# Optimization experiments

Measured on AMD Instinct MI355X. Metric: run time of the kernel, lower is better.

The kernel has to match this reference:

```python
import jax, jax.numpy as jnp
import numpy as np

HIGHWAY_BIAS = 0.0
# SRU rescale=True scales the highway residual to preserve variance:
# scale_x = sqrt(1 + exp(2*highway_bias)) = sqrt(2) for highway_bias=0
SCALE_X = float(np.sqrt(1.0 + np.exp(2.0 * HIGHWAY_BIAS)))
D = 128  # SRU hidden size


def sru_layer(x, W, v, b):
    """One SRU layer. x: (T,B,din); W: (din,k*D) with k=4 if din!=D else 3;
    v: (2,D) recurrent gate weights; b: (2,D) gate biases."""
    T, B, din = x.shape
    k = W.shape[1] // D
    U = jnp.einsum('tbi,ij->tbj', x, W).reshape(T, B, k, D)
    u0, u1, u2 = U[:, :, 0], U[:, :, 1], U[:, :, 2]
    res = U[:, :, 3] if k == 4 else x  # highway residual (projected if dims differ)
    vf, vr = v[0], v[1]
    bf, br = b[0], b[1]

    def step(c, inp):
        u0t, u1t, u2t, rt = inp
        f = jax.nn.sigmoid(u1t + vf * c + bf)          # forget gate (peeks at c_{t-1})
        c_new = f * c + (1.0 - f) * u0t                # cell update
        r = jax.nn.sigmoid(u2t + vr * c_new + br)      # reset/highway gate
        h = r * c_new + (1.0 - r) * rt * SCALE_X       # highway output
        return c_new, h

    c0 = jnp.zeros((B, D), x.dtype)
    _, h = jax.lax.scan(step, c0, (u0, u1, u2, res))
    return h  # (T,B,D)


def sru_stack(x, W0, v0, b0, W1, v1, b1):
    return sru_layer(sru_layer(x, W0, v0, b0), W1, v1, b1)


def setup_inputs() -> dict:
    key = jax.random.key(0)
    ks = jax.random.split(key, 20)
    B, T = 8, 32000
    s_in = 1.0 / np.sqrt(64.0)
    s_hid = 1.0 / np.sqrt(128.0)
    inp = {
        'tensor': jax.random.normal(ks[0], (B, 9, T), jnp.float32),
        'W_first': jax.random.normal(ks[1], (128, 9), jnp.float32) / 3.0,
        'b_first': jnp.zeros((128,), jnp.float32),
        'W_last': jax.random.normal(ks[2], (1, 128), jnp.float32) * s_hid,
        'b_last': jnp.zeros((1,), jnp.float32),
        # stack a = self.lstm2 (processes channels [:64])
        'a_W0': jax.random.normal(ks[3], (64, 4 * D), jnp.float32) * s_in,
        'a_v0': jax.random.normal(ks[4], (2, D), jnp.float32) * 0.1,
        'a_b0': jnp.zeros((2, D), jnp.float32),
        'a_W1': jax.random.normal(ks[5], (D, 3 * D), jnp.float32) * s_hid,
        'a_v1': jax.random.normal(ks[6], (2, D), jnp.float32) * 0.1,
        'a_b1': jnp.zeros((2, D), jnp.float32),
        # stack b = self.lstm (processes channels [64:])
        'b_W0': jax.random.normal(ks[7], (64, 4 * D), jnp.float32) * s_in,
        'b_v0': jax.random.normal(ks[8], (2, D), jnp.float32) * 0.1,
        'b_b0': jnp.zeros((2, D), jnp.float32),
        'b_W1': jax.random.normal(ks[9], (D, 3 * D), jnp.float32) * s_hid,
        'b_v1': jax.random.normal(ks[10], (2, D), jnp.float32) * 0.1,
        'b_b1': jnp.zeros((2, D), jnp.float32),
    }
    return inp


def reference(tensor, W_first, b_first, W_last, b_last,
              a_W0, a_v0, a_b0, a_W1, a_v1, a_b1,
              b_W0, b_v0, b_b0, b_W1, b_v1, b_b1):
    # first: Conv1d(9,128,1)
    h = jnp.einsum('oc,bct->bot', W_first, tensor) + b_first[None, :, None]  # (B,128,T)
    xa = jnp.transpose(h[:, :64], (2, 0, 1))   # (T,B,64) -> lstm2
    xb = jnp.transpose(h[:, 64:], (2, 0, 1))   # (T,B,64) -> lstm
    ya = sru_stack(xa, a_W0, a_v0, a_b0, a_W1, a_v1, a_b1)  # (T,B,128)
    yb = sru_stack(xb, b_W0, b_v0, b_b0, b_W1, b_v1, b_b1)
    s = jnp.transpose(ya + yb, (1, 2, 0))      # (B,128,T)
    # last: Conv1d(128,1,1)
    return jnp.einsum('oc,bct->bot', W_last, s) + b_last[None, :, None]  # (B,1,T)
```

## Files before the change

### kernel.cpp

```cpp
#include <hip/hip_runtime.h>
#include <hip/hip_bf16.h>

#define L2E   1.44269504088896340736f
#define SQRT2 1.41421356237309504880f

#define T_LEN 32000
#define BATCH 8
#define NCH   9

#define KCH0  125
#define CL0   256
#define WU    128
#define KCH1  32
#define CL1   1000
#define WUF   136
#define NTIL  71

#define MROWS (T_LEN*BATCH)

typedef __bf16 bf16x8 __attribute__((ext_vector_type(8)));
typedef float  f32x4  __attribute__((ext_vector_type(4)));
typedef float  f32x2  __attribute__((ext_vector_type(2)));

__global__ void prep_misc(const float* __restrict__ Wf, const float* __restrict__ bfirst,
                          const float* __restrict__ aW0, const float* __restrict__ bW0,
                          const float* __restrict__ ab0, const float* __restrict__ bb0,
                          const float* __restrict__ ab1, const float* __restrict__ bb1,
                          float* __restrict__ Mn, float* __restrict__ biasn,
                          float* __restrict__ bias1n) {
    int s = blockIdx.x, g = blockIdx.y;
    int d = threadIdx.x;
    const float* W0s = s ? bW0 : aW0;
    const float* b0s = s ? bb0 : ab0;
    const float* b1s = s ? bb1 : ab1;

    float scale = (g == 1 || g == 2) ? -L2E : (g == 3 ? SQRT2 : 1.0f);
    float bias = 0.f;
    for (int i = 0; i < 64; ++i) bias += bfirst[s*64 + i] * W0s[i*512 + g*128 + d];
    for (int c = 0; c < NCH; ++c) {
        float acc = 0.f;
        for (int i = 0; i < 64; ++i)
            acc += Wf[(s*64 + i)*NCH + c] * W0s[i*512 + g*128 + d];
        Mn[((s*NCH + c)*4 + g)*128 + d] = scale * acc;
    }
    float bb = bias;
    if (g == 1) bb = bias + b0s[d];
    if (g == 2) bb = bias + b0s[128 + d];
    biasn[(s*4 + g)*128 + d] = scale * bb;

    if (g == 0) {
        bias1n[s*384 + d      ] = 0.0f;
        bias1n[s*384 + 128 + d] = -L2E * b1s[d];
        bias1n[s*384 + 256 + d] = -L2E * b1s[128 + d];
    }
}

__global__ void prep_bpack(const float* __restrict__ aW1, const float* __restrict__ bW1,
                           __hip_bfloat16* __restrict__ Bpack) {
    int nt = blockIdx.x, s = blockIdx.y;
    int kt = threadIdx.x >> 6, lane = threadIdx.x & 63;
    const float* W1s = s ? bW1 : aW1;
    int n = nt*16 + (lane & 15);
    float csc = (n < 128) ? 1.0f : -L2E;
    for (int jj = 0; jj < 8; ++jj) {
        int k = kt*32 + (lane >> 4)*8 + jj;
        Bpack[((size_t)((s*24 + nt)*4 + kt)*64 + lane)*8 + jj] =
            __float2bfloat16(csc * W1s[k*384 + n]);
    }
}

__global__ __launch_bounds__(256, 4) void scan0(const float* __restrict__ tensor,
        const float* __restrict__ av0, const float* __restrict__ bv0,
        const float* __restrict__ Mn, const float* __restrict__ biasn,
        __hip_bfloat16* __restrict__ h0) {
    __shared__ __align__(16) float ldsx[(CL0 + WU) * 12];
    int chunk = blockIdx.x, b = blockIdx.y;
    int tid = threadIdx.x, wid = tid >> 6, lane = tid & 63;
    int s = wid >> 1, half = wid & 1, d = half*64 + lane;

    int t0 = chunk*CL0 - WU; if (t0 < 0) t0 = 0;
    int tend = (chunk + 1)*CL0;
    int nsteps = tend - t0;

    for (int c = 0; c < NCH; ++c) {
        const float* src = tensor + ((size_t)b*NCH + c)*T_LEN + t0;
        for (int j = tid; j < nsteps; j += 256) ldsx[j*12 + c] = src[j];
    }
    __syncthreads();

    f32x2 M01[NCH], M23[NCH], b01, b23;
    {
        float M[4][NCH], bi[4];
#pragma unroll
        for (int g = 0; g < 4; ++g) {
            bi[g] = biasn[(s*4 + g)*128 + d];
#pragma unroll
            for (int c = 0; c < NCH; ++c) M[g][c] = Mn[((s*NCH + c)*4 + g)*128 + d];
        }
#pragma unroll
        for (int c = 0; c < NCH; ++c) {
            M01[c] = (f32x2){M[0][c], M[1][c]};
            M23[c] = (f32x2){M[2][c], M[3][c]};
        }
        b01 = (f32x2){bi[0], bi[1]};
        b23 = (f32x2){bi[2], bi[3]};
    }
    const float* v0s = s ? bv0 : av0;
    float vf2 = -L2E * v0s[d];
    float vr2 = -L2E * v0s[128 + d];

    float cst = 0.f;
    int hw_off = chunk*CL0 - t0;
    __hip_bfloat16* hbase = h0 + ((size_t)s*MROWS + b)*128 + d;

    auto compU = [&](int grp, f32x2* u01v, f32x2* u23v) {
#pragma unroll
        for (int k = 0; k < 4; ++k) {
            const float* xr = ldsx + (grp*4 + k)*12;
            float4 xlo = *(const float4*)xr;
            float4 xhi = *(const float4*)(xr + 4);
            float x8 = xr[8];
            f32x2 a = b01, c2 = b23;
            a += M01[0]*xlo.x; c2 += M23[0]*xlo.x;
            a += M01[1]*xlo.y; c2 += M23[1]*xlo.y;
            a += M01[2]*xlo.z; c2 += M23[2]*xlo.z;
            a += M01[3]*xlo.w; c2 += M23[3]*xlo.w;
            a += M01[4]*xhi.x; c2 += M23[4]*xhi.x;
            a += M01[5]*xhi.y; c2 += M23[5]*xhi.y;
            a += M01[6]*xhi.z; c2 += M23[6]*xhi.z;
            a += M01[7]*xhi.w; c2 += M23[7]*xhi.w;
            a += M01[8]*x8;    c2 += M23[8]*x8;
            u01v[k] = a; u23v[k] = c2;
        }
    };
    auto chain = [&](f32x2* u01v, f32x2* u23v, int grp) {
#pragma unroll
        for (int k = 0; k < 4; ++k) {
            float e  = __builtin_amdgcn_exp2f(fmaf(vf2, cst, u01v[k].y));
            float g  = __builtin_amdgcn_rcpf(e + 1.0f);
            float cn = fmaf(g, cst - u01v[k].x, u01v[k].x);
            float er = __builtin_amdgcn_exp2f(fmaf(vr2, cn, u23v[k].x));
            float rr = __builtin_amdgcn_rcpf(er + 1.0f);
            float h  = fmaf(rr, cn - u23v[k].y, u23v[k].y);
            cst = cn;
            int j = grp*4 + k;
            if (j >= hw_off) hbase[(size_t)(t0 + j)*(BATCH*128)] = __float2bfloat16(h);
        }
    };

    f32x2 uA01[4], uA23[4], uB01[4], uB23[4];
    int ngrp = nsteps >> 2;
    compU(0, uA01, uA23);
    int g = 0;
    while (g + 2 <= ngrp) {
        compU(g + 1, uB01, uB23);
        chain(uA01, uA23, g);
        if (g + 2 < ngrp) compU(g + 2, uA01, uA23);
        chain(uB01, uB23, g + 1);
        g += 2;
    }
}

__global__ __launch_bounds__(768, 3) void scan1f(const __hip_bfloat16* __restrict__ h0,
        const __hip_bfloat16* __restrict__ Bpack, const float* __restrict__ bias1n,
        const float* __restrict__ av1, const float* __restrict__ bv1,
        const float* __restrict__ Wlast, float* __restrict__ pbuf) {
    __shared__ __align__(16) float ush[2][2][16][388];
    __shared__ unsigned int hstg[2][2][16][64];
    int chunk = blockIdx.x, b = blockIdx.y;
    int tid = threadIdx.x, wid = tid >> 6, lane = tid & 63;
    int cl = lane & 15, rsel = lane >> 4;
    int tw = chunk*CL1, t0 = tw - WUF;
    int pp = 0;

    if (wid >= 4) {
        int gw = wid - 4;
        int s_g = gw >> 2;
        int ntb = (gw & 3) * 6;
        bool hwr = ((gw & 3) == 0);
        bf16x8 Bfr[6][4];
        const bf16x8* bsrc = (const bf16x8*)Bpack;
#pragma unroll
        for (int i = 0; i < 6; ++i)
#pragma unroll
            for (int kt = 0; kt < 4; ++kt)
                Bfr[i][kt] = bsrc[((s_g*24 + ntb + i)*4 + kt)*64 + lane];
        float bias[6];
#pragma unroll
        for (int i = 0; i < 6; ++i) bias[i] = bias1n[s_g*384 + (ntb + i)*16 + cl];

        const __hip_bfloat16* habase = h0 + ((size_t)s_g*MROWS + b)*128 + rsel*8;
        bf16x8 A[4];
        auto loadA = [&](int tile) {
            int trow = t0 + tile*16 + cl; if (trow < 0) trow = 0;
            const __hip_bfloat16* ap = habase + (size_t)trow*(BATCH*128);
#pragma unroll
            for (int kt = 0; kt < 4; ++kt) A[kt] = *(const bf16x8*)(ap + kt*32);
        };
        auto gemmwrite = [&](int ppw) {
            f32x4 acc[6];
#pragma unroll
            for (int i = 0; i < 6; ++i) acc[i] = (f32x4){bias[i], bias[i], bias[i], bias[i]};
#pragma unroll
            for (int kt = 0; kt < 4; ++kt)
#pragma unroll
                for (int i = 0; i < 6; ++i)
                    acc[i] = __builtin_amdgcn_mfma_f32_16x16x32_bf16(A[kt], Bfr[i][kt], acc[i], 0, 0, 0);
            if (hwr) {
#pragma unroll
                for (int kt = 0; kt < 4; ++kt) {
                    uint4 aw = __builtin_bit_cast(uint4, A[kt]);
                    unsigned int* hrow = &hstg[ppw][s_g][cl][0];
                    hrow[(rsel*4 + kt*16 + 0) ^ cl] = aw.x;
                    hrow[(rsel*4 + kt*16 + 1) ^ cl] = aw.y;
                    hrow[(rsel*4 + kt*16 + 2) ^ cl] = aw.z;
                    hrow[(rsel*4 + kt*16 + 3) ^ cl] = aw.w;
                }
            }
#pragma unroll
            for (int i = 0; i < 6; ++i) {
                int col = (ntb + i)*16 + cl;
#pragma unroll
                for (int j = 0; j < 4; ++j)
                    ush[ppw][s_g][rsel*4 + j][col] = acc[i][j];
            }
        };
        loadA(0);
        gemmwrite(0);
        loadA(1);
        for (int tile = 0; tile < NTIL; ++tile) {
            __syncthreads();
            if (tile + 1 < NTIL) {
                gemmwrite(pp ^ 1);
                int tn = tile + 2; if (tn > NTIL - 1) tn = NTIL - 1;
                loadA(tn);
            }
            pp ^= 1;
        }
    } else {
        int s_s = wid >> 1, half = wid & 1, d = half*64 + lane;
        const float* v1s = s_s ? bv1 : av1;
        float vf2 = -L2E * v1s[d], vr2 = -L2E * v1s[128 + d];
        float wl = Wlast[d];
        float cst = 0.f;
        float* pb = pbuf + ((size_t)wid*BATCH + b)*T_LEN;
        int dsw = d >> 1, dodd = lane & 1;

        for (int tile = 0; tile < NTIL; ++tile) {
            __syncthreads();
            int tt0 = t0 + tile*16;
#pragma unroll
            for (int h8 = 0; h8 < 2; ++h8) {
                float u0v[8], u1v[8], u2v[8], rv[8], hv[8];
#pragma unroll
                for (int k = 0; k < 8; ++k) {
                    int tt = h8*8 + k;
                    const float* ur = &ush[pp][s_s][tt][0];
                    u0v[k] = ur[d]; u1v[k] = ur[128 + d]; u2v[k] = ur[256 + d];
                    unsigned int w = hstg[pp][s_s][tt][dsw ^ tt];
                    unsigned int hb = dodd ? (w >> 16) : (w & 0xffffu);
                    rv[k] = __uint_as_float(hb << 16);
                    if (tt0 + tt < 0) u1v[k] = -__builtin_inff();
                }
#pragma unroll
                for (int k = 0; k < 8; ++k) {
                    float e  = __builtin_amdgcn_exp2f(fmaf(vf2, cst, u1v[k]));
                    float g  = __builtin_amdgcn_rcpf(e + 1.0f);
                    float cn = fmaf(g, cst - u0v[k], u0v[k]);
                    float er = __builtin_amdgcn_exp2f(fmaf(vr2, cn, u2v[k]));
                    float rr = __builtin_amdgcn_rcpf(er + 1.0f);
                    float sr = SQRT2 * rv[k];
                    hv[k] = fmaf(rr, cn - sr, sr);
                    cst = cn;
                }
                float pr[8];
#pragma unroll
                for (int k = 0; k < 8; ++k) {
                    float p = wl * hv[k];
                    p += __shfl_xor(p, 32);
                    p += __shfl_xor(p, 16);
                    p += __shfl_xor(p, 8);
                    pr[k] = p;
                }
                int g3 = lane >> 3;
                float a0 = (g3 & 1) ? pr[1] : pr[0];
                float a1 = (g3 & 1) ? pr[3] : pr[2];
                float a2 = (g3 & 1) ? pr[5] : pr[4];
                float a3 = (g3 & 1) ? pr[7] : pr[6];
                float b0 = (g3 & 2) ? a1 : a0;
                float b1 = (g3 & 2) ? a3 : a2;
                float q  = (g3 & 4) ? b1 : b0;
                q += __shfl_xor(q, 1);
                q += __shfl_xor(q, 2);
                q += __shfl_xor(q, 4);
                int tsel = tt0 + h8*8 + g3;
                if ((lane & 7) == 0 && tsel >= tw) pb[tsel] = q;
            }
            pp ^= 1;
        }
    }
}

__global__ void finalk(const float* __restrict__ pbuf, const float* __restrict__ blast,
                       float* __restrict__ out) {
    int idx = blockIdx.x*256 + threadIdx.x;
    if (idx >= BATCH*T_LEN) return;
    int b = idx / T_LEN, t = idx - b*T_LEN;
    float v = blast[0];
#pragma unroll
    for (int k = 0; k < 4; ++k) v += pbuf[((size_t)k*BATCH + b)*T_LEN + t];
    out[idx] = v;
}

extern "C" void kernel_launch(void* const* d_in, const int* in_sizes, int n_in,
                              void* d_out, int out_size, void* d_ws, size_t ws_size,
                              hipStream_t stream) {
    const float* tensor = (const float*)d_in[0];
    const float* Wfirst = (const float*)d_in[1];
    const float* bfirst = (const float*)d_in[2];
    const float* Wlast  = (const float*)d_in[3];
    const float* blast  = (const float*)d_in[4];
    const float* aW0 = (const float*)d_in[5];
    const float* av0 = (const float*)d_in[6];
    const float* ab0 = (const float*)d_in[7];
    const float* aW1 = (const float*)d_in[8];
    const float* av1 = (const float*)d_in[9];
    const float* ab1 = (const float*)d_in[10];
    const float* bW0 = (const float*)d_in[11];
    const float* bv0 = (const float*)d_in[12];
    const float* bb0 = (const float*)d_in[13];
    const float* bW1 = (const float*)d_in[14];
    const float* bv1 = (const float*)d_in[15];
    const float* bb1 = (const float*)d_in[16];
    float* out = (float*)d_out;

    char* ws = (char*)d_ws;
    size_t off = 0;
    float* Mn     = (float*)(ws + off); off += 2*9*4*128*sizeof(float);
    float* biasn  = (float*)(ws + off); off += 2*4*128*sizeof(float);
    float* bias1n = (float*)(ws + off); off += 2*384*sizeof(float);
    off = (off + 255) & ~(size_t)255;
    __hip_bfloat16* Bpack = (__hip_bfloat16*)(ws + off); off += (size_t)2*24*4*64*8*2;
    off = (off + 255) & ~(size_t)255;
    float* pbuf = (float*)(ws + off); off += (size_t)4*BATCH*T_LEN*sizeof(float);
    off = (off + 255) & ~(size_t)255;
    __hip_bfloat16* h0 = (__hip_bfloat16*)(ws + off); off += (size_t)2*MROWS*128*2;
    (void)ws_size; (void)in_sizes; (void)n_in; (void)out_size;

    prep_misc<<<dim3(2, 4), 128, 0, stream>>>(Wfirst, bfirst, aW0, bW0, ab0, bb0, ab1, bb1,
                                              Mn, biasn, bias1n);
    prep_bpack<<<dim3(24, 2), 256, 0, stream>>>(aW1, bW1, Bpack);
    scan0<<<dim3(KCH0, BATCH), 256, 0, stream>>>(tensor, av0, bv0, Mn, biasn, h0);
    scan1f<<<dim3(KCH1, BATCH), 768, 0, stream>>>(h0, Bpack, bias1n, av1, bv1, Wlast, pbuf);
    finalk<<<dim3((BATCH*T_LEN + 255)/256), 256, 0, stream>>>(pbuf, blast, out);
}
```

Baseline: 457.3 us.

## Widen scan1f GEMM producers to 12 waves, double-buffer A, prioritize scan waves

scan1f now launches 1024 threads, so 12 producer waves each compute 4 N-tiles instead of 8 waves doing 6. A-fragment loads are double-buffered in two register sets so each load is issued a full tile ahead, and the scan waves get a raised scheduling priority. prep_misc stages Wf and bias in LDS and computes all 10 dot products in one pass, and scan0's occupancy hint drops from 4 to 3. The larger block increases per-CU register and LDS pressure, which could cut the number of resident blocks.

```diff
diff --git a/kernel.cpp b/kernel.cpp
--- a/kernel.cpp
+++ b/kernel.cpp
@@ -22,30 +22,42 @@
 typedef float  f32x4  __attribute__((ext_vector_type(4)));
 typedef float  f32x2  __attribute__((ext_vector_type(2)));
 
-__global__ void prep_misc(const float* __restrict__ Wf, const float* __restrict__ bfirst,
+__global__ __launch_bounds__(128) void prep_misc(const float* __restrict__ Wf,
+                          const float* __restrict__ bfirst,
                           const float* __restrict__ aW0, const float* __restrict__ bW0,
                           const float* __restrict__ ab0, const float* __restrict__ bb0,
                           const float* __restrict__ ab1, const float* __restrict__ bb1,
                           float* __restrict__ Mn, float* __restrict__ biasn,
                           float* __restrict__ bias1n) {
+    __shared__ float WfL[64][10];
     int s = blockIdx.x, g = blockIdx.y;
     int d = threadIdx.x;
     const float* W0s = s ? bW0 : aW0;
     const float* b0s = s ? bb0 : ab0;
     const float* b1s = s ? bb1 : ab1;
 
+    for (int idx = d; idx < 640; idx += 128) {
+        int i = idx / 10, c = idx - i*10;
+        WfL[i][c] = (c < NCH) ? Wf[(s*64 + i)*NCH + c] : bfirst[s*64 + i];
+    }
+    __syncthreads();
+
+    float acc[10];
+#pragma unroll
+    for (int c = 0; c < 10; ++c) acc[c] = 0.f;
+#pragma unroll 8
+    for (int i = 0; i < 64; ++i) {
+        float w = W0s[i*512 + g*128 + d];
+#pragma unroll
+        for (int c = 0; c < 10; ++c) acc[c] = fmaf(w, WfL[i][c], acc[c]);
+    }
     float scale = (g == 1 || g == 2) ? -L2E : (g == 3 ? SQRT2 : 1.0f);
-    float bias = 0.f;
-    for (int i = 0; i < 64; ++i) bias += bfirst[s*64 + i] * W0s[i*512 + g*128 + d];
-    for (int c = 0; c < NCH; ++c) {
-        float acc = 0.f;
-        for (int i = 0; i < 64; ++i)
-            acc += Wf[(s*64 + i)*NCH + c] * W0s[i*512 + g*128 + d];
-        Mn[((s*NCH + c)*4 + g)*128 + d] = scale * acc;
-    }
-    float bb = bias;
-    if (g == 1) bb = bias + b0s[d];
-    if (g == 2) bb = bias + b0s[128 + d];
+#pragma unroll
+    for (int c = 0; c < NCH; ++c)
+        Mn[((s*NCH + c)*4 + g)*128 + d] = scale * acc[c];
+    float bb = acc[9];
+    if (g == 1) bb += b0s[d];
+    if (g == 2) bb += b0s[128 + d];
     biasn[(s*4 + g)*128 + d] = scale * bb;
 
     if (g == 0) {
@@ -69,7 +81,7 @@
     }
 }
 
-__global__ __launch_bounds__(256, 4) void scan0(const float* __restrict__ tensor,
+__global__ __launch_bounds__(256, 3) void scan0(const float* __restrict__ tensor,
         const float* __restrict__ av0, const float* __restrict__ bv0,
         const float* __restrict__ Mn, const float* __restrict__ biasn,
         __hip_bfloat16* __restrict__ h0) {
@@ -161,7 +173,7 @@
     }
 }
 
-__global__ __launch_bounds__(768, 3) void scan1f(const __hip_bfloat16* __restrict__ h0,
+__global__ __launch_bounds__(1024, 4) void scan1f(const __hip_bfloat16* __restrict__ h0,
         const __hip_bfloat16* __restrict__ Bpack, const float* __restrict__ bias1n,
         const float* __restrict__ av1, const float* __restrict__ bv1,
         const float* __restrict__ Wlast, float* __restrict__ pbuf) {
@@ -175,37 +187,41 @@
 
     if (wid >= 4) {
         int gw = wid - 4;
-        int s_g = gw >> 2;
-        int ntb = (gw & 3) * 6;
-        bool hwr = ((gw & 3) == 0);
-        bf16x8 Bfr[6][4];
+        int s_g = (gw >= 6) ? 1 : 0;
+        int ntb = (gw - s_g*6) * 4;
+        bool hwr = (ntb == 0);
+        bf16x8 Bfr[4][4];
         const bf16x8* bsrc = (const bf16x8*)Bpack;
 #pragma unroll
-        for (int i = 0; i < 6; ++i)
+        for (int i = 0; i < 4; ++i)
 #pragma unroll
             for (int kt = 0; kt < 4; ++kt)
                 Bfr[i][kt] = bsrc[((s_g*24 + ntb + i)*4 + kt)*64 + lane];
-        float bias[6];
-#pragma unroll
-        for (int i = 0; i < 6; ++i) bias[i] = bias1n[s_g*384 + (ntb + i)*16 + cl];
+        float bias[4];
+#pragma unroll
+        for (int i = 0; i < 4; ++i) bias[i] = bias1n[s_g*384 + (ntb + i)*16 + cl];
 
         const __hip_bfloat16* habase = h0 + ((size_t)s_g*MROWS + b)*128 + rsel*8;
-        bf16x8 A[4];
-        auto loadA = [&](int tile) {
+        bf16x8 Aa[4], Ab[4];
+        auto loadA = [&](int tile, bf16x8 (&A)[4]) {
+            if (tile > NTIL - 1) tile = NTIL - 1;
             int trow = t0 + tile*16 + cl; if (trow < 0) trow = 0;
             const __hip_bfloat16* ap = habase + (size_t)trow*(BATCH*128);
 #pragma unroll
             for (int kt = 0; kt < 4; ++kt) A[kt] = *(const bf16x8*)(ap + kt*32);
         };
-        auto gemmwrite = [&](int ppw) {
-            f32x4 acc[6];
-#pragma unroll
-            for (int i = 0; i < 6; ++i) acc[i] = (f32x4){bias[i], bias[i], bias[i], bias[i]};
-#pragma unroll
-            for (int kt = 0; kt < 4; ++kt)
-#pragma unroll
-                for (int i = 0; i < 6; ++i)
-                    acc[i] = __builtin_amdgcn_mfma_f32_16x16x32_bf16(A[kt], Bfr[i][kt], acc[i], 0, 0, 0);
+        auto gemmwrite = [&](int ppw, bf16x8 (&A)[4]) {
+#pragma unroll
+            for (int i = 0; i < 4; ++i) {
+                f32x4 acc = (f32x4){bias[i], bias[i], bias[i], bias[i]};
+#pragma unroll
+                for (int kt = 0; kt < 4; ++kt)
+                    acc = __builtin_amdgcn_mfma_f32_16x16x32_bf16(A[kt], Bfr[i][kt], acc, 0, 0, 0);
+                int col = (ntb + i)*16 + cl;
+#pragma unroll
+                for (int j = 0; j < 4; ++j)
+                    ush[ppw][s_g][rsel*4 + j][col] = acc[j];
+            }
             if (hwr) {
 #pragma unroll
                 for (int kt = 0; kt < 4; ++kt) {
@@ -217,27 +233,23 @@
                     hrow[(rsel*4 + kt*16 + 3) ^ cl] = aw.w;
                 }
             }
-#pragma unroll
-            for (int i = 0; i < 6; ++i) {
-                int col = (ntb + i)*16 + cl;
-#pragma unroll
-                for (int j = 0; j < 4; ++j)
-                    ush[ppw][s_g][rsel*4 + j][col] = acc[i][j];
-            }
         };
-        loadA(0);
-        gemmwrite(0);
-        loadA(1);
-        for (int tile = 0; tile < NTIL; ++tile) {
+        loadA(0, Aa);
+        gemmwrite(0, Aa);
+        loadA(1, Ab);
+        for (int tile = 0; tile < NTIL - 1; tile += 2) {
             __syncthreads();
-            if (tile + 1 < NTIL) {
-                gemmwrite(pp ^ 1);
-                int tn = tile + 2; if (tn > NTIL - 1) tn = NTIL - 1;
-                loadA(tn);
-            }
+            loadA(tile + 2, Aa);
+            gemmwrite(pp ^ 1, Ab);
             pp ^= 1;
-        }
+            __syncthreads();
+            loadA(tile + 3, Ab);
+            if (tile + 2 < NTIL) gemmwrite(pp ^ 1, Aa);
+            pp ^= 1;
+        }
+        __syncthreads();
     } else {
+        __builtin_amdgcn_s_setprio(1);
         int s_s = wid >> 1, half = wid & 1, d = half*64 + lane;
         const float* v1s = s_s ? bv1 : av1;
         float vf2 = -L2E * v1s[d], vr2 = -L2E * v1s[128 + d];
@@ -351,6 +363,6 @@
                                               Mn, biasn, bias1n);
     prep_bpack<<<dim3(24, 2), 256, 0, stream>>>(aW1, bW1, Bpack);
     scan0<<<dim3(KCH0, BATCH), 256, 0, stream>>>(tensor, av0, bv0, Mn, biasn, h0);
-    scan1f<<<dim3(KCH1, BATCH), 768, 0, stream>>>(h0, Bpack, bias1n, av1, bv1, Wlast, pbuf);
+    scan1f<<<dim3(KCH1, BATCH), 1024, 0, stream>>>(h0, Bpack, bias1n, av1, bv1, Wlast, pbuf);
     finalk<<<dim3((BATCH*T_LEN + 255)/256), 256, 0, stream>>>(pbuf, blast, out);
 }
```

Result: faster. 427.1 us (-6.6%).
